# Kernel optimization log

Hardware: AMD Instinct MI355X
Metric: run time of the kernel (lower is better)

The kernel has to match this reference:

```python
import jax, jax.numpy as jnp
import numpy as np

EPS = 1e-09

def setup_inputs() -> dict:
    key = jax.random.key(0)
    k1, k2 = jax.random.split(key)
    N, C = 65536, 1024
    pred = jax.random.normal(k1, (N, C), dtype=jnp.float32)
    target = jax.random.randint(k2, (N,), 0, C, dtype=jnp.int64)
    return {"pred": pred, "target": target}

def reference(pred, target):
    # Faithful to the torch module: softmax over dim=0 (across the batch dim)
    p = jax.nn.softmax(pred, axis=0) + EPS  # epsilon added before BOTH log terms
    C = pred.shape[1]
    tar = jax.nn.one_hot(target, C, dtype=pred.dtype)  # [N, C]
    # per-row BCE with log base 2, mean over classes
    bce = tar * jnp.log2(p) + (1.0 - tar) * jnp.log2(1.0 - p)
    loss = -jnp.mean(bce, axis=1)  # [N]
    return jnp.mean(loss)
```

## Files before the change

### kernel.cpp

```cpp
#include <hip/hip_runtime.h>
#include <math.h>

static constexpr int N = 65536;
static constexpr int C = 1024;
static constexpr float EPS = 1e-9f;



template <int RPB>
__global__ __launch_bounds__(256) void colsum_partial_kernel(
    const float* __restrict__ pred, const int* __restrict__ tgt,
    float* __restrict__ partial, float* __restrict__ sxArr) {
    const int tid  = threadIdx.x;
    const int row0 = blockIdx.x * RPB;

    __shared__ int tgt_lds[RPB];
    if (tid < RPB) tgt_lds[tid] = tgt[row0 + tid];
    __syncthreads();

    const float4* __restrict__ p4 =
        reinterpret_cast<const float4*>(pred) + (size_t)row0 * (C / 4) + tid;

    float a0 = 0.f, a1 = 0.f, a2 = 0.f, a3 = 0.f;
    float sx = 0.f;
#pragma unroll 1
    for (int b = 0; b < RPB / 8; ++b) {
        float4 v0 = p4[0 * (C / 4)];
        float4 v1 = p4[1 * (C / 4)];
        float4 v2 = p4[2 * (C / 4)];
        float4 v3 = p4[3 * (C / 4)];
        float4 v4 = p4[4 * (C / 4)];
        float4 v5 = p4[5 * (C / 4)];
        float4 v6 = p4[6 * (C / 4)];
        float4 v7 = p4[7 * (C / 4)];
        p4 += 8 * (C / 4);
        __builtin_amdgcn_sched_barrier(0);

#pragma unroll
        for (int r = 0; r < 8; ++r) {
            const int tc = tgt_lds[b * 8 + r];
            if ((tc >> 2) == tid) {
                const float4 v = (r == 0) ? v0 : (r == 1) ? v1 : (r == 2) ? v2
                               : (r == 3) ? v3 : (r == 4) ? v4 : (r == 5) ? v5
                               : (r == 6) ? v6 : v7;
                const int sel = tc & 3;
                sx += (sel == 0) ? v.x : (sel == 1) ? v.y : (sel == 2) ? v.z : v.w;
            }
        }

        a0 += __expf(v0.x) + __expf(v1.x) + __expf(v2.x) + __expf(v3.x)
            + __expf(v4.x) + __expf(v5.x) + __expf(v6.x) + __expf(v7.x);
        a1 += __expf(v0.y) + __expf(v1.y) + __expf(v2.y) + __expf(v3.y)
            + __expf(v4.y) + __expf(v5.y) + __expf(v6.y) + __expf(v7.y);
        a2 += __expf(v0.z) + __expf(v1.z) + __expf(v2.z) + __expf(v3.z)
            + __expf(v4.z) + __expf(v5.z) + __expf(v6.z) + __expf(v7.z);
        a3 += __expf(v0.w) + __expf(v1.w) + __expf(v2.w) + __expf(v3.w)
            + __expf(v4.w) + __expf(v5.w) + __expf(v6.w) + __expf(v7.w);
    }

    reinterpret_cast<float4*>(partial + (size_t)blockIdx.x * C)[tid] =
        make_float4(a0, a1, a2, a3);

#pragma unroll
    for (int off = 32; off > 0; off >>= 1)
        sx += __shfl_down(sx, off, 64);
    __shared__ float wsum[4];
    if ((tid & 63) == 0) wsum[tid >> 6] = sx;
    __syncthreads();
    if (tid == 0)
        sxArr[blockIdx.x] = wsum[0] + wsum[1] + wsum[2] + wsum[3];
}

__global__ __launch_bounds__(256) void colsum_reduce_kernel(
    const float* __restrict__ partial, float* __restrict__ S, int rows) {
    const int c = blockIdx.x * 256 + threadIdx.x;
    const float* __restrict__ p = partial + (size_t)blockIdx.y * rows * C + c;
    float s0 = 0.f, s1 = 0.f, s2 = 0.f, s3 = 0.f,
          s4 = 0.f, s5 = 0.f, s6 = 0.f, s7 = 0.f;
    for (int r = 0; r < rows; r += 8) {
        s0 += p[0 * C]; s1 += p[1 * C]; s2 += p[2 * C]; s3 += p[3 * C];
        s4 += p[4 * C]; s5 += p[5 * C]; s6 += p[6 * C]; s7 += p[7 * C];
        p += 8 * C;
    }
    atomicAdd(&S[c], ((s0 + s1) + (s2 + s3)) + ((s4 + s5) + (s6 + s7)));
}

__global__ __launch_bounds__(256) void tgt_log_kernel(
    const int* __restrict__ tgt, const float* __restrict__ S,
    float* __restrict__ accL) {
    const int n = blockIdx.x * 256 + threadIdx.x;
    float v = log2f(S[tgt[n]]);
#pragma unroll
    for (int off = 32; off > 0; off >>= 1)
        v += __shfl_down(v, off, 64);
    __shared__ float wsum[4];
    if ((threadIdx.x & 63) == 0) wsum[threadIdx.x >> 6] = v;
    __syncthreads();
    if (threadIdx.x == 0)
        atomicAdd(accL, wsum[0] + wsum[1] + wsum[2] + wsum[3]);
}

__global__ __launch_bounds__(256) void finalize_kernel(
    const float* __restrict__ sxArr, int RB, const float* __restrict__ accL,
    float* __restrict__ out) {
    float s = 0.f;
    for (int i = threadIdx.x; i < RB; i += 256) s += sxArr[i];
#pragma unroll
    for (int off = 32; off > 0; off >>= 1)
        s += __shfl_down(s, off, 64);
    __shared__ float wsum[4];
    if ((threadIdx.x & 63) == 0) wsum[threadIdx.x >> 6] = s;
    __syncthreads();
    if (threadIdx.x == 0) {
        const double LOG2E = 1.4426950408889634;
        double sumX = (double)(wsum[0] + wsum[1] + wsum[2] + wsum[3]);
        double termA = -LOG2E * (double)C * (1.0 + (double)N * (double)EPS);
        double total = termA + LOG2E * sumX - (double)accL[0];
        out[0] = (float)(-total / ((double)N * (double)C));
    }
}

extern "C" void kernel_launch(void* const* d_in, const int* in_sizes, int n_in,
                              void* d_out, int out_size, void* d_ws, size_t ws_size,
                              hipStream_t stream) {
    const float* pred = (const float*)d_in[0];
    const int*   tgt  = (const int*)d_in[1];
    float* S       = (float*)d_ws;
    float* accL    = S + C;
    float* sxArr   = S + 1032;
    float* partial = S + 4096;
    const size_t base_bytes = 4096 * sizeof(float);

    int RB = 2048;
    while (RB > 512 && base_bytes + (size_t)RB * C * sizeof(float) > ws_size)
        RB >>= 1;

    hipMemsetAsync(d_ws, 0, (C + 8) * sizeof(float), stream);

    if (RB >= 2048)
        colsum_partial_kernel<32><<<2048, 256, 0, stream>>>(pred, tgt, partial, sxArr);
    else if (RB == 1024)
        colsum_partial_kernel<64><<<1024, 256, 0, stream>>>(pred, tgt, partial, sxArr);
    else
        colsum_partial_kernel<128><<<512, 256, 0, stream>>>(pred, tgt, partial, sxArr);

    const int GY = 32;
    colsum_reduce_kernel<<<dim3(C / 256, GY), 256, 0, stream>>>(partial, S, RB / GY);
    tgt_log_kernel<<<N / 256, 256, 0, stream>>>(tgt, S, accL);
    finalize_kernel<<<1, 256, 0, stream>>>(sxArr, RB, accL, (float*)d_out);
}
```

Baseline: 65.84 us.

## Fuse column reduce, target gather and finalize into one last-block kernel

Replaces the memset, the atomic column reduce, the per-row log gather and the finalize kernels with a single kernel. Each of 64 blocks reduces 16 columns of the partial sums and writes log2 of them. The last block to finish, found through an atomic counter, loads those logs into LDS, gathers them by target and finishes the scalar result. The counter is reset inside the first kernel so the memset is no longer needed. This cuts launch overhead and global atomics, but the final gather over 65536 targets now runs serially in one block and the reduce uses only 64 blocks.

```diff
diff --git a/kernel.cpp b/kernel.cpp
--- a/kernel.cpp
+++ b/kernel.cpp
@@ -6,13 +6,14 @@
 static constexpr float EPS = 1e-9f;
 
 
-
 template <int RPB>
 __global__ __launch_bounds__(256) void colsum_partial_kernel(
     const float* __restrict__ pred, const int* __restrict__ tgt,
-    float* __restrict__ partial, float* __restrict__ sxArr) {
+    float* __restrict__ partial, float* __restrict__ sxArr,
+    int* __restrict__ counter) {
     const int tid  = threadIdx.x;
     const int row0 = blockIdx.x * RPB;
+    if (blockIdx.x == 0 && tid == 0) *counter = 0;
 
     __shared__ int tgt_lds[RPB];
     if (tid < RPB) tgt_lds[tid] = tgt[row0 + tid];
@@ -71,51 +72,91 @@
         sxArr[blockIdx.x] = wsum[0] + wsum[1] + wsum[2] + wsum[3];
 }
 
-__global__ __launch_bounds__(256) void colsum_reduce_kernel(
-    const float* __restrict__ partial, float* __restrict__ S, int rows) {
-    const int c = blockIdx.x * 256 + threadIdx.x;
-    const float* __restrict__ p = partial + (size_t)blockIdx.y * rows * C + c;
-    float s0 = 0.f, s1 = 0.f, s2 = 0.f, s3 = 0.f,
-          s4 = 0.f, s5 = 0.f, s6 = 0.f, s7 = 0.f;
-    for (int r = 0; r < rows; r += 8) {
-        s0 += p[0 * C]; s1 += p[1 * C]; s2 += p[2 * C]; s3 += p[3 * C];
-        s4 += p[4 * C]; s5 += p[5 * C]; s6 += p[6 * C]; s7 += p[7 * C];
-        p += 8 * C;
+__global__ __launch_bounds__(256) void reduce_gather_kernel(
+    const float* __restrict__ partial, const int* __restrict__ tgt,
+    const float* __restrict__ sxArr, float* __restrict__ logS,
+    int* __restrict__ counter, float* __restrict__ out, int RB) {
+    const int t  = threadIdx.x;
+    const int cp = t & 7;
+    const int r0 = t >> 3;
+    const int c0 = blockIdx.x * 16;
+    const int eighth = RB / 8;
+
+    const float2* __restrict__ p2 =
+        reinterpret_cast<const float2*>(partial) + (c0 >> 1) + cp;
+
+    float2 a[8];
+#pragma unroll
+    for (int j = 0; j < 8; ++j) a[j] = make_float2(0.f, 0.f);
+    for (int r = r0; r < eighth; r += 32) {
+#pragma unroll
+        for (int j = 0; j < 8; ++j) {
+            const float2 v = p2[(size_t)(r + j * eighth) * (C / 2)];
+            a[j].x += v.x;
+            a[j].y += v.y;
+        }
     }
-    atomicAdd(&S[c], ((s0 + s1) + (s2 + s3)) + ((s4 + s5) + (s6 + s7)));
-}
+    float2 s;
+    s.x = ((a[0].x + a[1].x) + (a[2].x + a[3].x)) + ((a[4].x + a[5].x) + (a[6].x + a[7].x));
+    s.y = ((a[0].y + a[1].y) + (a[2].y + a[3].y)) + ((a[4].y + a[5].y) + (a[6].y + a[7].y));
+#pragma unroll
+    for (int off = 8; off <= 32; off <<= 1) {
+        s.x += __shfl_xor(s.x, off, 64);
+        s.y += __shfl_xor(s.y, off, 64);
+    }
+    __shared__ float2 wred[4][8];
+    if ((t & 63) < 8) wred[t >> 6][cp] = s;
+    __syncthreads();
+    if (t < 8) {
+        const float vx = wred[0][t].x + wred[1][t].x + wred[2][t].x + wred[3][t].x;
+        const float vy = wred[0][t].y + wred[1][t].y + wred[2][t].y + wred[3][t].y;
+        __hip_atomic_store(&logS[c0 + 2 * t],     log2f(vx),
+                           __ATOMIC_RELEASE, __HIP_MEMORY_SCOPE_AGENT);
+        __hip_atomic_store(&logS[c0 + 2 * t + 1], log2f(vy),
+                           __ATOMIC_RELEASE, __HIP_MEMORY_SCOPE_AGENT);
+        __threadfence();
+    }
+    __syncthreads();
 
-__global__ __launch_bounds__(256) void tgt_log_kernel(
-    const int* __restrict__ tgt, const float* __restrict__ S,
-    float* __restrict__ accL) {
-    const int n = blockIdx.x * 256 + threadIdx.x;
-    float v = log2f(S[tgt[n]]);
+    __shared__ int last;
+    if (t == 0) {
+        const int old = __hip_atomic_fetch_add(counter, 1, __ATOMIC_ACQ_REL,
+                                               __HIP_MEMORY_SCOPE_AGENT);
+        last = (old == (int)gridDim.x - 1) ? 1 : 0;
+    }
+    __syncthreads();
+    if (!last) return;
+
+    __shared__ float lut[C];
+    for (int i = t; i < C; i += 256)
+        lut[i] = __hip_atomic_load(&logS[i], __ATOMIC_RELAXED,
+                                   __HIP_MEMORY_SCOPE_AGENT);
+    __syncthreads();
+
+    float accL = 0.f;
+    for (int n = t; n < N; n += 256 * 8) {
+        accL += lut[tgt[n + 256 * 0]] + lut[tgt[n + 256 * 1]]
+              + lut[tgt[n + 256 * 2]] + lut[tgt[n + 256 * 3]]
+              + lut[tgt[n + 256 * 4]] + lut[tgt[n + 256 * 5]]
+              + lut[tgt[n + 256 * 6]] + lut[tgt[n + 256 * 7]];
+    }
+    float sx = 0.f;
+    for (int i = t; i < RB; i += 256) sx += sxArr[i];
+
 #pragma unroll
-    for (int off = 32; off > 0; off >>= 1)
-        v += __shfl_down(v, off, 64);
-    __shared__ float wsum[4];
-    if ((threadIdx.x & 63) == 0) wsum[threadIdx.x >> 6] = v;
+    for (int off = 32; off > 0; off >>= 1) {
+        accL += __shfl_down(accL, off, 64);
+        sx   += __shfl_down(sx, off, 64);
+    }
+    __shared__ float r1[4], r2[4];
+    if ((t & 63) == 0) { r1[t >> 6] = accL; r2[t >> 6] = sx; }
     __syncthreads();
-    if (threadIdx.x == 0)
-        atomicAdd(accL, wsum[0] + wsum[1] + wsum[2] + wsum[3]);
-}
-
-__global__ __launch_bounds__(256) void finalize_kernel(
-    const float* __restrict__ sxArr, int RB, const float* __restrict__ accL,
-    float* __restrict__ out) {
-    float s = 0.f;
-    for (int i = threadIdx.x; i < RB; i += 256) s += sxArr[i];
-#pragma unroll
-    for (int off = 32; off > 0; off >>= 1)
-        s += __shfl_down(s, off, 64);
-    __shared__ float wsum[4];
-    if ((threadIdx.x & 63) == 0) wsum[threadIdx.x >> 6] = s;
-    __syncthreads();
-    if (threadIdx.x == 0) {
+    if (t == 0) {
         const double LOG2E = 1.4426950408889634;
-        double sumX = (double)(wsum[0] + wsum[1] + wsum[2] + wsum[3]);
-        double termA = -LOG2E * (double)C * (1.0 + (double)N * (double)EPS);
-        double total = termA + LOG2E * sumX - (double)accL[0];
+        const double SumLogS = (double)(r1[0] + r1[1] + r1[2] + r1[3]);
+        const double SumX    = (double)(r2[0] + r2[1] + r2[2] + r2[3]);
+        const double termA   = -LOG2E * (double)C * (1.0 + (double)N * (double)EPS);
+        const double total   = termA + LOG2E * SumX - SumLogS;
         out[0] = (float)(-total / ((double)N * (double)C));
     }
 }
@@ -125,27 +166,24 @@
                               hipStream_t stream) {
     const float* pred = (const float*)d_in[0];
     const int*   tgt  = (const int*)d_in[1];
-    float* S       = (float*)d_ws;
-    float* accL    = S + C;
-    float* sxArr   = S + 1032;
-    float* partial = S + 4096;
+    float* wsf     = (float*)d_ws;
+    float* logS    = wsf;
+    int*   counter = (int*)(wsf + 1024);
+    float* sxArr   = wsf + 1088;
+    float* partial = wsf + 4096;
     const size_t base_bytes = 4096 * sizeof(float);
 
     int RB = 2048;
     while (RB > 512 && base_bytes + (size_t)RB * C * sizeof(float) > ws_size)
         RB >>= 1;
 
-    hipMemsetAsync(d_ws, 0, (C + 8) * sizeof(float), stream);
+    if (RB >= 2048)
+        colsum_partial_kernel<32><<<2048, 256, 0, stream>>>(pred, tgt, partial, sxArr, counter);
+    else if (RB == 1024)
+        colsum_partial_kernel<64><<<1024, 256, 0, stream>>>(pred, tgt, partial, sxArr, counter);
+    else
+        colsum_partial_kernel<128><<<512, 256, 0, stream>>>(pred, tgt, partial, sxArr, counter);
 
-    if (RB >= 2048)
-        colsum_partial_kernel<32><<<2048, 256, 0, stream>>>(pred, tgt, partial, sxArr);
-    else if (RB == 1024)
-        colsum_partial_kernel<64><<<1024, 256, 0, stream>>>(pred, tgt, partial, sxArr);
-    else
-        colsum_partial_kernel<128><<<512, 256, 0, stream>>>(pred, tgt, partial, sxArr);
-
-    const int GY = 32;
-    colsum_reduce_kernel<<<dim3(C / 256, GY), 256, 0, stream>>>(partial, S, RB / GY);
-    tgt_log_kernel<<<N / 256, 256, 0, stream>>>(tgt, S, accL);
-    finalize_kernel<<<1, 256, 0, stream>>>(sxArr, RB, accL, (float*)d_out);
+    reduce_gather_kernel<<<64, 256, 0, stream>>>(partial, tgt, sxArr, logS,
+                                                 counter, (float*)d_out, RB);
 }
```

Result: slower. 71.77 us (+9.0%).
